# Optimization experiments

Hardware: AMD Instinct MI355X
Metric: run time of the kernel (lower is better)

Reference implementation:

```python
import jax, jax.numpy as jnp
from jax import lax
import numpy as np

BALANCE = 1.0  # polynomial kernel: (conv(x,w)+b + BALANCE)**POWER
POWER = 2


def _conv(x, w, b, stride, pad):
    y = lax.conv_general_dilated(
        x, w, window_strides=(stride, stride),
        padding=[(pad, pad), (pad, pad)],
        dimension_numbers=('NCHW', 'OIHW', 'NCHW'))
    return y + b[None, :, None, None]


def kerv2d(x, w, b, stride, pad):
    # PolyKervNets degree-2 polynomial kervolution
    y = _conv(x, w, b, stride, pad) + BALANCE
    return y * y  # (.)**2


def avgpool3s2(x):
    s = lax.reduce_window(x, 0.0, lax.add, (1, 1, 3, 3), (1, 1, 2, 2), 'VALID')
    return s * (1.0 / 9.0)


def setup_inputs() -> dict:
    key = jax.random.key(0)
    ks = jax.random.split(key, 17)
    sc = 0.01  # small init so repeated squaring stays numerically sane
    d = {}
    d['x'] = jax.random.normal(ks[0], (64, 3, 227, 227), jnp.float32)
    d['w1'] = jax.random.normal(ks[1], (96, 3, 11, 11), jnp.float32) * sc
    d['b1'] = jnp.zeros((96,), jnp.float32)
    d['w2'] = jax.random.normal(ks[2], (256, 96, 5, 5), jnp.float32) * sc
    d['b2'] = jnp.zeros((256,), jnp.float32)
    d['w3'] = jax.random.normal(ks[3], (384, 256, 3, 3), jnp.float32) * sc
    d['b3'] = jnp.zeros((384,), jnp.float32)
    d['w4'] = jax.random.normal(ks[4], (384, 384, 3, 3), jnp.float32) * sc
    d['b4'] = jnp.zeros((384,), jnp.float32)
    d['w5'] = jax.random.normal(ks[5], (256, 384, 3, 3), jnp.float32) * sc
    d['b5'] = jnp.zeros((256,), jnp.float32)
    d['fw1'] = jax.random.normal(ks[6], (9216, 4096), jnp.float32) * sc
    d['fb1'] = jnp.zeros((4096,), jnp.float32)
    d['fw2'] = jax.random.normal(ks[7], (4096, 4096), jnp.float32) * sc
    d['fb2'] = jnp.zeros((4096,), jnp.float32)
    d['fw3'] = jax.random.normal(ks[8], (4096, 1000), jnp.float32) * sc
    d['fb3'] = jnp.zeros((1000,), jnp.float32)
    return d


def reference(x, w1, b1, w2, b2, w3, b3, w4, b4, w5, b5,
              fw1, fb1, fw2, fb2, fw3, fb3):
    x = kerv2d(x, w1, b1, stride=4, pad=0)   # [B,96,55,55]
    x = avgpool3s2(x)                        # [B,96,27,27]
    x = kerv2d(x, w2, b2, stride=1, pad=2)   # [B,256,27,27]
    x = avgpool3s2(x)                        # [B,256,13,13]
    x = kerv2d(x, w3, b3, stride=1, pad=1)   # [B,384,13,13]
    x = kerv2d(x, w4, b4, stride=1, pad=1)   # [B,384,13,13]
    x = kerv2d(x, w5, b5, stride=1, pad=1)   # [B,256,13,13]
    x = avgpool3s2(x)                        # [B,256,6,6]
    x = x.reshape(x.shape[0], -1)            # [B,9216]
    x = x @ fw1 + fb1
    x = x @ fw2 + fb2
    x = x @ fw3 + fb3
    return x
```

## Files before the change

### kernel.cpp

```cpp
#include <hip/hip_runtime.h>


typedef _Float16 f16;
typedef _Float16 f16x8 __attribute__((ext_vector_type(8)));
typedef float    f32x4 __attribute__((ext_vector_type(4)));

#define CDIV(a,b) (((a)+(b)-1)/(b))
#define SWZ(row,g) ((g) ^ (((row) >> 2) & 3))

template<int C,int H,int W,int OC,int R,int S,int PAD,int STRIDE,int OH,int OW,
         int KRUN,int BM,int BN>
__global__ __launch_bounds__(256)
void conv_mfma(const f16* __restrict__ in, const f16* __restrict__ wt,
               const float* __restrict__ bias, f16* __restrict__ out)
{
    constexpr int KTOT = (KRUN > 0) ? (R * KRUN) : (C * R * S);
    constexpr int KP   = (KTOT + 31) & ~31;
    constexpr int OHW  = OH * OW;
    constexpr int NTOT = 64 * OHW;
    constexpr int AM   = BM / 32;
    constexpr int AN   = BN / 32;
    constexpr int AU   = BM * 4 / 256;
    constexpr int BU   = BN * 4 / 256;

    __shared__ __align__(16) f16 As[BM * 32];
    __shared__ __align__(16) f16 Bs[BN * 32];

    const int t   = threadIdx.x;
    const int n0  = blockIdx.x * BN;
    const int oc0 = blockIdx.y * BM;

    int a_row[AU], a_g[AU], a_lds[AU]; bool a_ok[AU];
    #pragma unroll
    for (int i = 0; i < AU; ++i) {
        const int u = t + i * 256;
        a_row[i] = u >> 2;
        a_g[i]   = u & 3;
        a_lds[i] = a_row[i] * 32 + SWZ(a_row[i], a_g[i]) * 8;
        a_ok[i]  = (oc0 + a_row[i]) < OC;
    }
    int b_row[BU], b_g[BU], b_lds[BU], b_img[BU], b_oy[BU], b_ox[BU]; bool b_ok[BU];
    #pragma unroll
    for (int i = 0; i < BU; ++i) {
        const int u = t + i * 256;
        b_row[i] = u >> 2;
        b_g[i]   = u & 3;
        b_lds[i] = b_row[i] * 32 + SWZ(b_row[i], b_g[i]) * 8;
        const int n   = n0 + b_row[i];
        b_ok[i]       = n < NTOT;
        const int ncl = b_ok[i] ? n : 0;
        b_img[i] = ncl / OHW;
        const int rem = ncl - b_img[i] * OHW;
        b_oy[i]  = rem / OW;
        b_ox[i]  = rem - b_oy[i] * OW;
    }

    const int wv = t >> 6;
    const int wm = (wv >> 1) * (BM / 2);
    const int wn = (wv & 1) * (BN / 2);
    const int l  = t & 63;
    const int il = l & 15;
    const int q  = l >> 4;

    f32x4 acc[AM][AN];
    #pragma unroll
    for (int i = 0; i < AM; ++i)
        #pragma unroll
        for (int j = 0; j < AN; ++j)
            acc[i][j] = (f32x4){0.f, 0.f, 0.f, 0.f};

    int4 aReg[AU], bReg[BU];

    auto loadA = [&](int kc) {
        #pragma unroll
        for (int i = 0; i < AU; ++i) {
            int4 v = {0, 0, 0, 0};
            if (a_ok[i])
                v = *(const int4*)(wt + (size_t)(oc0 + a_row[i]) * KP + kc + a_g[i] * 8);
            aReg[i] = v;
        }
    };
    auto loadB = [&](int kc) {
        #pragma unroll
        for (int i = 0; i < BU; ++i) {
            if constexpr (KRUN > 0) {
                const int k8 = kc + b_g[i] * 8;
                const int r  = k8 / KRUN;
                const int j0 = k8 - r * KRUN;
                int4 v = {0, 0, 0, 0};
                if (b_ok[i] && k8 < KTOT) {
                    const f16* p = in + ((size_t)(b_img[i] * H + b_oy[i] * STRIDE + r) * W
                                         + b_ox[i] * STRIDE) * C + j0;
                    const int2 lo = *(const int2*)p;
                    const int2 hi = *(const int2*)(p + 4);
                    v.x = lo.x; v.y = lo.y; v.z = hi.x; v.w = hi.y;
                }
                bReg[i] = v;
            } else {
                const int k8 = kc + b_g[i] * 8;
                const int rs = k8 / C;
                const int c0 = k8 - rs * C;
                const int r  = rs / S;
                const int s  = rs - r * S;
                const int iy = b_oy[i] * STRIDE + r - PAD;
                const int ix = b_ox[i] * STRIDE + s - PAD;
                int4 v = {0, 0, 0, 0};
                if (b_ok[i] && iy >= 0 && iy < H && ix >= 0 && ix < W)
                    v = *(const int4*)(in + ((size_t)(b_img[i] * H + iy) * W + ix) * C + c0);
                bReg[i] = v;
            }
        }
    };

    loadA(0); loadB(0);

    for (int kc = 0; kc < KP; kc += 32) {
        #pragma unroll
        for (int i = 0; i < AU; ++i) *(int4*)&As[a_lds[i]] = aReg[i];
        #pragma unroll
        for (int i = 0; i < BU; ++i) *(int4*)&Bs[b_lds[i]] = bReg[i];
        __syncthreads();

        if (kc + 32 < KP) { loadA(kc + 32); loadB(kc + 32); }

        f16x8 af[AM], bf[AN];
        #pragma unroll
        for (int mi = 0; mi < AM; ++mi) {
            const int row = wm + mi * 16 + il;
            af[mi] = *(const f16x8*)&As[row * 32 + SWZ(row, q) * 8];
        }
        #pragma unroll
        for (int ni = 0; ni < AN; ++ni) {
            const int row = wn + ni * 16 + il;
            bf[ni] = *(const f16x8*)&Bs[row * 32 + SWZ(row, q) * 8];
        }
        #pragma unroll
        for (int mi = 0; mi < AM; ++mi)
            #pragma unroll
            for (int ni = 0; ni < AN; ++ni)
                acc[mi][ni] = __builtin_amdgcn_mfma_f32_16x16x32_f16(
                    af[mi], bf[ni], acc[mi][ni], 0, 0, 0);
        __syncthreads();
    }

    #pragma unroll
    for (int mi = 0; mi < AM; ++mi) {
        const int ocb = oc0 + wm + mi * 16 + q * 4;
        if (ocb >= OC) continue;
        const float4 bb = *(const float4*)(bias + ocb);
        const float b4[4] = {bb.x + 1.f, bb.y + 1.f, bb.z + 1.f, bb.w + 1.f};
        #pragma unroll
        for (int ni = 0; ni < AN; ++ni) {
            const int nn = n0 + wn + ni * 16 + il;
            if (nn >= NTOT) continue;
            const f32x4 v = acc[mi][ni];
            union { f16 h[4]; uint2 u; } cv;
            const float vv[4] = {v.x, v.y, v.z, v.w};
            #pragma unroll
            for (int rr = 0; rr < 4; ++rr) {
                const float y = vv[rr] + b4[rr];
                cv.h[rr] = (f16)(y * y);
            }
            *(uint2*)(out + (size_t)nn * OC + ocb) = cv.u;
        }
    }
}

template<bool TAIL>
__global__ __launch_bounds__(256)
void fc_mfma2(const f16* __restrict__ X, const float* __restrict__ Wm,
              float* __restrict__ P, int N, int Npad, int K, int kchunk)
{
    __shared__ __align__(16) f16 Xs[64 * 32];
    __shared__ __align__(16) f16 Ws[256 * 32];

    const int t  = threadIdx.x;
    const int n0 = blockIdx.x * 256;
    const int s  = blockIdx.y;
    const int k0 = s * kchunk;
    const int nIter = kchunk / 32;

    const bool wok = !TAIL || (n0 + t) < N;
    const float* __restrict__ wbase = Wm + (size_t)k0 * N + n0 + t;
    const int xm = t >> 2;
    const int xg = t & 3;
    const f16* __restrict__ xbase = X + (size_t)xm * K + k0 + xg * 8;
    const int xoff = xm * 32 + SWZ(xm, xg) * 8;

    const int wq = t >> 6;
    const int l  = t & 63;
    const int il = l & 15;
    const int q  = l >> 4;

    f32x4 acc[4][4];
    #pragma unroll
    for (int i = 0; i < 4; ++i)
        #pragma unroll
        for (int j = 0; j < 4; ++j)
            acc[i][j] = (f32x4){0.f, 0.f, 0.f, 0.f};

    float wreg[4][8];
    int4  xreg;

    auto loadChunk = [&](int it) {
        const size_t kbase = (size_t)it * 32;
        #pragma unroll
        for (int g = 0; g < 4; ++g)
            #pragma unroll
            for (int j = 0; j < 8; ++j)
                wreg[g][j] = wok ? wbase[(kbase + g * 8 + j) * N] : 0.f;
        xreg = *(const int4*)(xbase + kbase);
    };

    loadChunk(0);

    for (int it = 0; it < nIter; ++it) {
        #pragma unroll
        for (int g = 0; g < 4; ++g) {
            f16x8 h;
            #pragma unroll
            for (int j = 0; j < 8; ++j) h[j] = (f16)wreg[g][j];
            *(f16x8*)&Ws[t * 32 + SWZ(t, g) * 8] = h;
        }
        *(int4*)&Xs[xoff] = xreg;
        __syncthreads();

        if (it + 1 < nIter) loadChunk(it + 1);

        f16x8 af[4], bf[4];
        #pragma unroll
        for (int mi = 0; mi < 4; ++mi) {
            const int m = mi * 16 + il;
            af[mi] = *(const f16x8*)&Xs[m * 32 + SWZ(m, q) * 8];
        }
        #pragma unroll
        for (int ni = 0; ni < 4; ++ni) {
            const int n = wq * 64 + ni * 16 + il;
            bf[ni] = *(const f16x8*)&Ws[n * 32 + SWZ(n, q) * 8];
        }
        #pragma unroll
        for (int mi = 0; mi < 4; ++mi)
            #pragma unroll
            for (int ni = 0; ni < 4; ++ni)
                acc[mi][ni] = __builtin_amdgcn_mfma_f32_16x16x32_f16(
                    af[mi], bf[ni], acc[mi][ni], 0, 0, 0);
        __syncthreads();
    }

    float* __restrict__ pb = P + (size_t)s * 64 * Npad + n0;
    #pragma unroll
    for (int mi = 0; mi < 4; ++mi) {
        const int m = mi * 16 + q * 4;
        #pragma unroll
        for (int ni = 0; ni < 4; ++ni) {
            const int n = wq * 64 + ni * 16 + il;
            const f32x4 v = acc[mi][ni];
            const float vv[4] = {v.x, v.y, v.z, v.w};
            #pragma unroll
            for (int rr = 0; rr < 4; ++rr)
                pb[(size_t)(m + rr) * Npad + n] = vv[rr];
        }
    }
}

template<bool F16OUT>
__global__ __launch_bounds__(256)
void fc_reduce(const float* __restrict__ P, const float* __restrict__ bias,
               f16* __restrict__ o16, float* __restrict__ o32,
               int N, int Npad, int S)
{
    const int idx = blockIdx.x * 256 + threadIdx.x;
    const int total = 64 * (N / 4);
    if (idx >= total) return;
    const int n4 = (idx % (N / 4)) * 4;
    const int m  = idx / (N / 4);
    float4 a = *(const float4*)(bias + n4);
    const float* __restrict__ p = P + (size_t)m * Npad + n4;
    for (int s = 0; s < S; ++s) {
        const float4 v = *(const float4*)(p + (size_t)s * 64 * Npad);
        a.x += v.x; a.y += v.y; a.z += v.z; a.w += v.w;
    }
    if (F16OUT) {
        union { f16 h[4]; uint2 u; } cv;
        cv.h[0] = (f16)a.x; cv.h[1] = (f16)a.y;
        cv.h[2] = (f16)a.z; cv.h[3] = (f16)a.w;
        *(uint2*)(o16 + (size_t)m * N + n4) = cv.u;
    } else {
        *(float4*)(o32 + (size_t)m * N + n4) = a;
    }
}

__global__ __launch_bounds__(256)
void avgpool_nhwc8(const f16* __restrict__ in, f16* __restrict__ out,
                   int C8, int C, int H, int W, int OH, int OW, int total8)
{
    const int idx = blockIdx.x * 256 + threadIdx.x;
    if (idx >= total8) return;
    const int c8  = (idx % C8) * 8;
    int rest      = idx / C8;
    const int ox  = rest % OW; rest /= OW;
    const int oy  = rest % OH;
    const int b   = rest / OH;
    const f16* __restrict__ p = in + ((size_t)(b * H + oy * 2) * W + ox * 2) * C + c8;
    float s[8] = {0.f, 0.f, 0.f, 0.f, 0.f, 0.f, 0.f, 0.f};
    #pragma unroll
    for (int r = 0; r < 3; ++r)
        #pragma unroll
        for (int cc = 0; cc < 3; ++cc) {
            const f16x8 v = *(const f16x8*)&p[(r * W + cc) * C];
            #pragma unroll
            for (int j = 0; j < 8; ++j) s[j] += (float)v[j];
        }
    f16x8 o8;
    #pragma unroll
    for (int j = 0; j < 8; ++j) o8[j] = (f16)(s[j] * (1.f / 9.f));
    *(f16x8*)(out + (size_t)idx * 8) = o8;
}

__global__ __launch_bounds__(256)
void pool5_ncflat(const f16* __restrict__ in, f16* __restrict__ out)
{
    const int idx = blockIdx.x * 256 + threadIdx.x;
    if (idx >= 64 * 6 * 6 * 256) return;
    const int c  = idx & 255;
    int rest     = idx >> 8;
    const int ox = rest % 6; rest /= 6;
    const int oy = rest % 6;
    const int b  = rest / 6;
    const f16* __restrict__ p = in + ((size_t)(b * 13 + oy * 2) * 13 + ox * 2) * 256 + c;
    float s = 0.f;
    #pragma unroll
    for (int r = 0; r < 3; ++r)
        #pragma unroll
        for (int cc = 0; cc < 3; ++cc)
            s += (float)p[(r * 13 + cc) * 256];
    out[(size_t)b * 9216 + c * 36 + oy * 6 + ox] = (f16)(s * (1.f / 9.f));
}

__global__ __launch_bounds__(256)
void x_to_nhwc4(const float* __restrict__ x, f16* __restrict__ o)
{
    const int idx = blockIdx.x * 256 + threadIdx.x;
    if (idx >= 64 * 227 * 227) return;
    const int hw = idx % (227 * 227);
    const int b  = idx / (227 * 227);
    const size_t plane = 227 * 227;
    const float* __restrict__ p = x + (size_t)b * 3 * plane + hw;
    union { f16 h[4]; int2 v; } u;
    u.h[0] = (f16)p[0];
    u.h[1] = (f16)p[plane];
    u.h[2] = (f16)p[2 * plane];
    u.h[3] = (f16)0.f;
    *(int2*)(o + (size_t)idx * 4) = u.v;
}

__global__ __launch_bounds__(256)
void wt_tf1(const float* __restrict__ w, f16* __restrict__ o)
{
    const int idx = blockIdx.x * 256 + threadIdx.x;
    if (idx >= 96 * 544) return;
    const int k  = idx % 544;
    const int oc = idx / 544;
    f16 v = (f16)0.f;
    if (k < 528) {
        const int r   = k / 48;
        const int rem = k - r * 48;
        const int s   = rem >> 2;
        const int c   = rem & 3;
        if (s < 11 && c < 3)
            v = (f16)w[(((size_t)oc * 3 + c) * 11 + r) * 11 + s];
    }
    o[idx] = v;
}

__global__ __launch_bounds__(256)
void wt_tf(const float* __restrict__ w, f16* __restrict__ o,
           int OC, int Cc, int R, int S, int KP)
{
    const int idx = blockIdx.x * 256 + threadIdx.x;
    if (idx >= OC * KP) return;
    const int k  = idx % KP;
    const int oc = idx / KP;
    f16 v = (f16)0.f;
    if (k < Cc * R * S) {
        const int rs = k / Cc;
        const int c  = k - rs * Cc;
        const int r  = rs / S;
        const int s  = rs - r * S;
        v = (f16)w[(((size_t)oc * Cc + c) * R + r) * S + s];
    }
    o[idx] = v;
}

extern "C" void kernel_launch(void* const* d_in, const int* in_sizes, int n_in,
                              void* d_out, int out_size, void* d_ws, size_t ws_size,
                              hipStream_t stream)
{
    const float* x   = (const float*)d_in[0];
    const float* w1  = (const float*)d_in[1];
    const float* b1  = (const float*)d_in[2];
    const float* w2  = (const float*)d_in[3];
    const float* b2  = (const float*)d_in[4];
    const float* w3  = (const float*)d_in[5];
    const float* b3  = (const float*)d_in[6];
    const float* w4  = (const float*)d_in[7];
    const float* b4  = (const float*)d_in[8];
    const float* w5  = (const float*)d_in[9];
    const float* b5  = (const float*)d_in[10];
    const float* fw1 = (const float*)d_in[11];
    const float* fb1 = (const float*)d_in[12];
    const float* fw2 = (const float*)d_in[13];
    const float* fb2 = (const float*)d_in[14];
    const float* fw3 = (const float*)d_in[15];
    const float* fb3 = (const float*)d_in[16];
    float* out = (float*)d_out;

    char* ws = (char*)d_ws;
    const size_t MiB = 1024 * 1024;

    f16*   X0  = (f16*)(ws);
    float* P   = (float*)(ws);
    f16*   Xh1 = (f16*)(ws + 17 * MiB);
    f16*   Xh2 = (f16*)(ws + 19 * MiB);
    f16*   Xh3 = (f16*)(ws + 20 * MiB);
    f16*   A   = (f16*)(ws + 26 * MiB);
    f16*   Bp  = (f16*)(ws + 62 * MiB);
    f16*   Wt1 = (f16*)(ws + 72 * MiB);
    f16*   Wt2 = Wt1 + (size_t)96  * 544;
    f16*   Wt3 = Wt2 + (size_t)256 * 2400;
    f16*   Wt4 = Wt3 + (size_t)384 * 2304;
    f16*   Wt5 = Wt4 + (size_t)384 * 3456;

    wt_tf1<<<CDIV(96 * 544, 256), 256, 0, stream>>>(w1, Wt1);
    wt_tf<<<CDIV(256 * 2400, 256), 256, 0, stream>>>(w2, Wt2, 256, 96 , 5, 5, 2400);
    wt_tf<<<CDIV(384 * 2304, 256), 256, 0, stream>>>(w3, Wt3, 384, 256, 3, 3, 2304);
    wt_tf<<<CDIV(384 * 3456, 256), 256, 0, stream>>>(w4, Wt4, 384, 384, 3, 3, 3456);
    wt_tf<<<CDIV(256 * 3456, 256), 256, 0, stream>>>(w5, Wt5, 256, 384, 3, 3, 3456);

    x_to_nhwc4<<<CDIV(64 * 227 * 227, 256), 256, 0, stream>>>(x, X0);

    conv_mfma<4,227,227,96,11,11,0,4,55,55,48,128,128>
        <<<dim3(CDIV(64 * 55 * 55, 128), 1), 256, 0, stream>>>(X0, Wt1, b1, A);
    {
        const int total8 = 64 * 27 * 27 * (96 / 8);
        avgpool_nhwc8<<<CDIV(total8, 256), 256, 0, stream>>>(A, Bp, 96 / 8, 96, 55, 55, 27, 27, total8);
    }
    conv_mfma<96,27,27,256,5,5,2,1,27,27,0,128,128>
        <<<dim3(CDIV(64 * 27 * 27, 128), 2), 256, 0, stream>>>(Bp, Wt2, b2, A);
    {
        const int total8 = 64 * 13 * 13 * (256 / 8);
        avgpool_nhwc8<<<CDIV(total8, 256), 256, 0, stream>>>(A, Bp, 256 / 8, 256, 27, 27, 13, 13, total8);
    }
    conv_mfma<256,13,13,384,3,3,1,1,13,13,0,128,64>
        <<<dim3(169, 3), 256, 0, stream>>>(Bp, Wt3, b3, A);
    conv_mfma<384,13,13,384,3,3,1,1,13,13,0,128,64>
        <<<dim3(169, 3), 256, 0, stream>>>(A, Wt4, b4, Bp);
    conv_mfma<384,13,13,256,3,3,1,1,13,13,0,128,64>
        <<<dim3(169, 2), 256, 0, stream>>>(Bp, Wt5, b5, A);

    pool5_ncflat<<<CDIV(64 * 6 * 6 * 256, 256), 256, 0, stream>>>(A, Xh1);

    fc_mfma2<false><<<dim3(16, 16), 256, 0, stream>>>(Xh1, fw1, P, 4096, 4096, 9216, 576);
    fc_reduce<true><<<CDIV(64 * 4096 / 4, 256), 256, 0, stream>>>(P, fb1, Xh2, nullptr, 4096, 4096, 16);
    fc_mfma2<false><<<dim3(16, 16), 256, 0, stream>>>(Xh2, fw2, P, 4096, 4096, 4096, 256);
    fc_reduce<true><<<CDIV(64 * 4096 / 4, 256), 256, 0, stream>>>(P, fb2, Xh3, nullptr, 4096, 4096, 16);
    fc_mfma2<true><<<dim3(4, 64), 256, 0, stream>>>(Xh3, fw3, P, 1000, 1024, 4096, 64);
    fc_reduce<false><<<CDIV(64 * 1000 / 4, 256), 256, 0, stream>>>(P, fb3, nullptr, out, 1000, 1024, 64);
}
```

Baseline: 689.7 us.

## Store activations in zero-padded NHWC buffers to drop im2col bounds checks

Producers (the avgpool and conv epilogues) now write their outputs into spatially padded NHWC buffers whose borders are zeroed by a new border_zero kernel. The implicit-GEMM B loader therefore walks a precomputed pointer with incremental offsets, replacing per-chunk div/mod and bounds checks. The A loader also loses its per-load row validity test by clamping the row pointer once. This adds extra small kernel launches, a reorganised workspace layout and slightly larger intermediate buffers.

```diff
diff --git a/kernel.cpp b/kernel.cpp
--- a/kernel.cpp
+++ b/kernel.cpp
@@ -8,20 +8,23 @@
 #define CDIV(a,b) (((a)+(b)-1)/(b))
 #define SWZ(row,g) ((g) ^ (((row) >> 2) & 3))
 
-template<int C,int H,int W,int OC,int R,int S,int PAD,int STRIDE,int OH,int OW,
-         int KRUN,int BM,int BN>
+template<int C,int HP,int WP,int OC,int R,int S,int STRIDE,int OH,int OW,
+         int OPAD,int KRUN,int BM,int BN>
 __global__ __launch_bounds__(256)
 void conv_mfma(const f16* __restrict__ in, const f16* __restrict__ wt,
                const float* __restrict__ bias, f16* __restrict__ out)
 {
     constexpr int KTOT = (KRUN > 0) ? (R * KRUN) : (C * R * S);
     constexpr int KP   = (KTOT + 31) & ~31;
+    static_assert(KRUN > 0 || KP == KTOT, "padded path requires K % 32 == 0");
     constexpr int OHW  = OH * OW;
     constexpr int NTOT = 64 * OHW;
     constexpr int AM   = BM / 32;
     constexpr int AN   = BN / 32;
     constexpr int AU   = BM * 4 / 256;
     constexpr int BU   = BN * 4 / 256;
+    constexpr int HPo  = OH + 2 * OPAD;
+    constexpr int WPo  = OW + 2 * OPAD;
 
     __shared__ __align__(16) f16 As[BM * 32];
     __shared__ __align__(16) f16 Bs[BN * 32];
@@ -30,29 +33,33 @@
     const int n0  = blockIdx.x * BN;
     const int oc0 = blockIdx.y * BM;
 
-    int a_row[AU], a_g[AU], a_lds[AU]; bool a_ok[AU];
+    int a_lds[AU]; const f16* aptr[AU];
     #pragma unroll
     for (int i = 0; i < AU; ++i) {
-        const int u = t + i * 256;
-        a_row[i] = u >> 2;
-        a_g[i]   = u & 3;
-        a_lds[i] = a_row[i] * 32 + SWZ(a_row[i], a_g[i]) * 8;
-        a_ok[i]  = (oc0 + a_row[i]) < OC;
-    }
-    int b_row[BU], b_g[BU], b_lds[BU], b_img[BU], b_oy[BU], b_ox[BU]; bool b_ok[BU];
+        const int u   = t + i * 256;
+        const int row = u >> 2;
+        const int g   = u & 3;
+        a_lds[i] = row * 32 + SWZ(row, g) * 8;
+        const int rowc = (oc0 + row < OC) ? (oc0 + row) : 0;
+        aptr[i] = wt + (size_t)rowc * KP + g * 8;
+    }
+    int b_lds[BU], b_g[BU], b_img[BU], b_oy[BU], b_ox[BU]; bool b_ok[BU];
+    const f16* bptr[BU];
     #pragma unroll
     for (int i = 0; i < BU; ++i) {
-        const int u = t + i * 256;
-        b_row[i] = u >> 2;
+        const int u   = t + i * 256;
+        const int row = u >> 2;
         b_g[i]   = u & 3;
-        b_lds[i] = b_row[i] * 32 + SWZ(b_row[i], b_g[i]) * 8;
-        const int n   = n0 + b_row[i];
+        b_lds[i] = row * 32 + SWZ(row, b_g[i]) * 8;
+        const int n   = n0 + row;
         b_ok[i]       = n < NTOT;
         const int ncl = b_ok[i] ? n : 0;
         b_img[i] = ncl / OHW;
         const int rem = ncl - b_img[i] * OHW;
         b_oy[i]  = rem / OW;
         b_ox[i]  = rem - b_oy[i] * OW;
+        bptr[i]  = in + ((size_t)(b_img[i] * HP + b_oy[i] * STRIDE) * WP
+                         + b_ox[i] * STRIDE) * C + b_g[i] * 8;
     }
 
     const int wv = t >> 6;
@@ -73,46 +80,38 @@
 
     auto loadA = [&](int kc) {
         #pragma unroll
-        for (int i = 0; i < AU; ++i) {
-            int4 v = {0, 0, 0, 0};
-            if (a_ok[i])
-                v = *(const int4*)(wt + (size_t)(oc0 + a_row[i]) * KP + kc + a_g[i] * 8);
-            aReg[i] = v;
-        }
+        for (int i = 0; i < AU; ++i)
+            aReg[i] = *(const int4*)(aptr[i] + kc);
     };
-    auto loadB = [&](int kc) {
-        #pragma unroll
-        for (int i = 0; i < BU; ++i) {
-            if constexpr (KRUN > 0) {
+    auto loadBp = [&](int koff) {
+        #pragma unroll
+        for (int i = 0; i < BU; ++i)
+            bReg[i] = *(const int4*)(bptr[i] + koff);
+    };
+    auto loadB1 = [&](int kc) {
+        if constexpr (KRUN > 0) {
+            #pragma unroll
+            for (int i = 0; i < BU; ++i) {
                 const int k8 = kc + b_g[i] * 8;
                 const int r  = k8 / KRUN;
                 const int j0 = k8 - r * KRUN;
                 int4 v = {0, 0, 0, 0};
                 if (b_ok[i] && k8 < KTOT) {
-                    const f16* p = in + ((size_t)(b_img[i] * H + b_oy[i] * STRIDE + r) * W
+                    const f16* p = in + ((size_t)(b_img[i] * HP + b_oy[i] * STRIDE + r) * WP
                                          + b_ox[i] * STRIDE) * C + j0;
                     const int2 lo = *(const int2*)p;
                     const int2 hi = *(const int2*)(p + 4);
                     v.x = lo.x; v.y = lo.y; v.z = hi.x; v.w = hi.y;
                 }
                 bReg[i] = v;
-            } else {
-                const int k8 = kc + b_g[i] * 8;
-                const int rs = k8 / C;
-                const int c0 = k8 - rs * C;
-                const int r  = rs / S;
-                const int s  = rs - r * S;
-                const int iy = b_oy[i] * STRIDE + r - PAD;
-                const int ix = b_ox[i] * STRIDE + s - PAD;
-                int4 v = {0, 0, 0, 0};
-                if (b_ok[i] && iy >= 0 && iy < H && ix >= 0 && ix < W)
-                    v = *(const int4*)(in + ((size_t)(b_img[i] * H + iy) * W + ix) * C + c0);
-                bReg[i] = v;
             }
         }
     };
 
-    loadA(0); loadB(0);
+    loadA(0);
+    if constexpr (KRUN > 0) loadB1(0); else loadBp(0);
+
+    int ks = 0, kcb = 0, koff = 0;
 
     for (int kc = 0; kc < KP; kc += 32) {
         #pragma unroll
@@ -121,7 +120,19 @@
         for (int i = 0; i < BU; ++i) *(int4*)&Bs[b_lds[i]] = bReg[i];
         __syncthreads();
 
-        if (kc + 32 < KP) { loadA(kc + 32); loadB(kc + 32); }
+        if (kc + 32 < KP) {
+            loadA(kc + 32);
+            if constexpr (KRUN > 0) {
+                loadB1(kc + 32);
+            } else {
+                koff += 32; kcb += 32;
+                if (kcb == C) {
+                    kcb = 0;
+                    if (++ks == S) { ks = 0; koff += (WP - S) * C; }
+                }
+                loadBp(koff);
+            }
+        }
 
         f16x8 af[AM], bf[AN];
         #pragma unroll
@@ -143,6 +154,18 @@
         __syncthreads();
     }
 
+    size_t noff[AN]; bool nok[AN];
+    #pragma unroll
+    for (int ni = 0; ni < AN; ++ni) {
+        const int nn = n0 + wn + ni * 16 + il;
+        nok[ni] = nn < NTOT;
+        const int ncl = nok[ni] ? nn : 0;
+        const int img = ncl / OHW;
+        const int rem = ncl - img * OHW;
+        const int oy  = rem / OW;
+        const int ox  = rem - oy * OW;
+        noff[ni] = ((size_t)(img * HPo + oy + OPAD) * WPo + (ox + OPAD)) * OC;
+    }
     #pragma unroll
     for (int mi = 0; mi < AM; ++mi) {
         const int ocb = oc0 + wm + mi * 16 + q * 4;
@@ -151,8 +174,7 @@
         const float b4[4] = {bb.x + 1.f, bb.y + 1.f, bb.z + 1.f, bb.w + 1.f};
         #pragma unroll
         for (int ni = 0; ni < AN; ++ni) {
-            const int nn = n0 + wn + ni * 16 + il;
-            if (nn >= NTOT) continue;
+            if (!nok[ni]) continue;
             const f32x4 v = acc[mi][ni];
             union { f16 h[4]; uint2 u; } cv;
             const float vv[4] = {v.x, v.y, v.z, v.w};
@@ -161,7 +183,7 @@
                 const float y = vv[rr] + b4[rr];
                 cv.h[rr] = (f16)(y * y);
             }
-            *(uint2*)(out + (size_t)nn * OC + ocb) = cv.u;
+            *(uint2*)(out + noff[ni] + ocb) = cv.u;
         }
     }
 }
@@ -292,7 +314,8 @@
 
 __global__ __launch_bounds__(256)
 void avgpool_nhwc8(const f16* __restrict__ in, f16* __restrict__ out,
-                   int C8, int C, int H, int W, int OH, int OW, int total8)
+                   int C8, int C, int H, int W, int OH, int OW,
+                   int HPo, int WPo, int opad, int total8)
 {
     const int idx = blockIdx.x * 256 + threadIdx.x;
     if (idx >= total8) return;
@@ -314,7 +337,21 @@
     f16x8 o8;
     #pragma unroll
     for (int j = 0; j < 8; ++j) o8[j] = (f16)(s[j] * (1.f / 9.f));
-    *(f16x8*)(out + (size_t)idx * 8) = o8;
+    *(f16x8*)(out + ((size_t)(b * HPo + oy + opad) * WPo + (ox + opad)) * C + c8) = o8;
+}
+
+__global__ __launch_bounds__(256)
+void border_zero(f16* __restrict__ buf, int HPb, int WPb, int C8, int pad,
+                 int total8)
+{
+    const int idx = blockIdx.x * 256 + threadIdx.x;
+    if (idx >= total8) return;
+    int rest = idx / C8;
+    const int x = rest % WPb; rest /= WPb;
+    const int y = rest % HPb;
+    if (y >= pad && y < HPb - pad && x >= pad && x < WPb - pad) return;
+    const int4 z = {0, 0, 0, 0};
+    *(int4*)(buf + (size_t)idx * 8) = z;
 }
 
 __global__ __launch_bounds__(256)
@@ -418,18 +455,23 @@
     char* ws = (char*)d_ws;
     const size_t MiB = 1024 * 1024;
 
-    f16*   X0  = (f16*)(ws);
-    float* P   = (float*)(ws);
-    f16*   Xh1 = (f16*)(ws + 17 * MiB);
-    f16*   Xh2 = (f16*)(ws + 19 * MiB);
-    f16*   Xh3 = (f16*)(ws + 20 * MiB);
-    f16*   A   = (f16*)(ws + 26 * MiB);
-    f16*   Bp  = (f16*)(ws + 62 * MiB);
-    f16*   Wt1 = (f16*)(ws + 72 * MiB);
+    f16*   Wt1 = (f16*)(ws);
     f16*   Wt2 = Wt1 + (size_t)96  * 544;
     f16*   Wt3 = Wt2 + (size_t)256 * 2400;
     f16*   Wt4 = Wt3 + (size_t)384 * 2304;
     f16*   Wt5 = Wt4 + (size_t)384 * 3456;
+    f16*   Xh1 = (f16*)(ws + 8  * MiB);
+    f16*   Xh2 = (f16*)(ws + 10 * MiB);
+    f16*   Xh3 = (f16*)(ws + 11 * MiB);
+    f16*   X0  = (f16*)(ws + 12 * MiB);
+    f16*   A2  = (f16*)(ws + 12 * MiB);
+    float* P   = (float*)(ws + 12 * MiB);
+    f16*   Bp3 = (f16*)(ws + 35 * MiB);
+    f16*   A1  = (f16*)(ws + 43 * MiB);
+    f16*   A4  = (f16*)(ws + 43 * MiB);
+    f16*   Bp5 = (f16*)(ws + 54 * MiB);
+    f16*   A5  = (f16*)(ws + 65 * MiB);
+    f16*   Bp2 = (f16*)(ws + 79 * MiB);
 
     wt_tf1<<<CDIV(96 * 544, 256), 256, 0, stream>>>(w1, Wt1);
     wt_tf<<<CDIV(256 * 2400, 256), 256, 0, stream>>>(w2, Wt2, 256, 96 , 5, 5, 2400);
@@ -438,27 +480,30 @@
     wt_tf<<<CDIV(256 * 3456, 256), 256, 0, stream>>>(w5, Wt5, 256, 384, 3, 3, 3456);
 
     x_to_nhwc4<<<CDIV(64 * 227 * 227, 256), 256, 0, stream>>>(x, X0);
-
-    conv_mfma<4,227,227,96,11,11,0,4,55,55,48,128,128>
-        <<<dim3(CDIV(64 * 55 * 55, 128), 1), 256, 0, stream>>>(X0, Wt1, b1, A);
-    {
-        const int total8 = 64 * 27 * 27 * (96 / 8);
-        avgpool_nhwc8<<<CDIV(total8, 256), 256, 0, stream>>>(A, Bp, 96 / 8, 96, 55, 55, 27, 27, total8);
-    }
-    conv_mfma<96,27,27,256,5,5,2,1,27,27,0,128,128>
-        <<<dim3(CDIV(64 * 27 * 27, 128), 2), 256, 0, stream>>>(Bp, Wt2, b2, A);
-    {
-        const int total8 = 64 * 13 * 13 * (256 / 8);
-        avgpool_nhwc8<<<CDIV(total8, 256), 256, 0, stream>>>(A, Bp, 256 / 8, 256, 27, 27, 13, 13, total8);
-    }
-    conv_mfma<256,13,13,384,3,3,1,1,13,13,0,128,64>
-        <<<dim3(169, 3), 256, 0, stream>>>(Bp, Wt3, b3, A);
-    conv_mfma<384,13,13,384,3,3,1,1,13,13,0,128,64>
-        <<<dim3(169, 3), 256, 0, stream>>>(A, Wt4, b4, Bp);
-    conv_mfma<384,13,13,256,3,3,1,1,13,13,0,128,64>
-        <<<dim3(169, 2), 256, 0, stream>>>(Bp, Wt5, b5, A);
-
-    pool5_ncflat<<<CDIV(64 * 6 * 6 * 256, 256), 256, 0, stream>>>(A, Xh1);
+    border_zero<<<CDIV(64 * 31 * 31 * 12, 256), 256, 0, stream>>>(Bp2, 31, 31, 12, 2, 64 * 31 * 31 * 12);
+
+    conv_mfma<4,227,227,96,11,11,4,55,55,0,48,128,128>
+        <<<dim3(CDIV(64 * 55 * 55, 128), 1), 256, 0, stream>>>(X0, Wt1, b1, A1);
+    avgpool_nhwc8<<<CDIV(64 * 27 * 27 * 12, 256), 256, 0, stream>>>(
+        A1, Bp2, 12, 96, 55, 55, 27, 27, 31, 31, 2, 64 * 27 * 27 * 12);
+
+    border_zero<<<CDIV(64 * 15 * 15 * 32, 256), 256, 0, stream>>>(Bp3, 15, 15, 32, 1, 64 * 15 * 15 * 32);
+    border_zero<<<CDIV(64 * 15 * 15 * 48, 256), 256, 0, stream>>>(A4 , 15, 15, 48, 1, 64 * 15 * 15 * 48);
+    border_zero<<<CDIV(64 * 15 * 15 * 48, 256), 256, 0, stream>>>(Bp5, 15, 15, 48, 1, 64 * 15 * 15 * 48);
+
+    conv_mfma<96,31,31,256,5,5,1,27,27,0,0,128,128>
+        <<<dim3(CDIV(64 * 27 * 27, 128), 2), 256, 0, stream>>>(Bp2, Wt2, b2, A2);
+    avgpool_nhwc8<<<CDIV(64 * 13 * 13 * 32, 256), 256, 0, stream>>>(
+        A2, Bp3, 32, 256, 27, 27, 13, 13, 15, 15, 1, 64 * 13 * 13 * 32);
+
+    conv_mfma<256,15,15,384,3,3,1,13,13,1,0,128,64>
+        <<<dim3(169, 3), 256, 0, stream>>>(Bp3, Wt3, b3, A4);
+    conv_mfma<384,15,15,384,3,3,1,13,13,1,0,128,64>
+        <<<dim3(169, 3), 256, 0, stream>>>(A4, Wt4, b4, Bp5);
+    conv_mfma<384,15,15,256,3,3,1,13,13,0,0,128,64>
+        <<<dim3(169, 2), 256, 0, stream>>>(Bp5, Wt5, b5, A5);
+
+    pool5_ncflat<<<CDIV(64 * 6 * 6 * 256, 256), 256, 0, stream>>>(A5, Xh1);
 
     fc_mfma2<false><<<dim3(16, 16), 256, 0, stream>>>(Xh1, fw1, P, 4096, 4096, 9216, 576);
     fc_reduce<true><<<CDIV(64 * 4096 / 4, 256), 256, 0, stream>>>(P, fb1, Xh2, nullptr, 4096, 4096, 16);
```

Measured after the change: 1.030 ms. 49.3% more time.
